# Performance work log

Measured on AMD Instinct MI355X. Metric: run time of the kernel, lower is better.

The kernel has to match this reference:

```python
import jax, jax.numpy as jnp
import numpy as np

EPS = 1e-08  # attention offset, matches module epsilon


def _ln(x, g, b, eps=1e-5):
    m = jnp.mean(x, axis=-1, keepdims=True)
    v = jnp.var(x, axis=-1, keepdims=True)
    return (x - m) * jax.lax.rsqrt(v + eps) * g + b


def setup_inputs() -> dict:
    key = jax.random.key(0)
    ks = jax.random.split(key, 12)
    B, N, D, S, H = 32, 16384, 64, 7, 128
    sc = 1.0 / np.sqrt(D)
    sch = 1.0 / np.sqrt(H)
    return {
        "inputs": jax.random.normal(ks[0], (B, N, D), jnp.float32),
        "ln_in_g": jnp.ones((D,), jnp.float32), "ln_in_b": jnp.zeros((D,), jnp.float32),
        "ln_slots_g": jnp.ones((D,), jnp.float32), "ln_slots_b": jnp.zeros((D,), jnp.float32),
        "ln_mlp_g": jnp.ones((D,), jnp.float32), "ln_mlp_b": jnp.zeros((D,), jnp.float32),
        "Wq": jax.random.normal(ks[1], (D, D), jnp.float32) * sc,
        "Wk": jax.random.normal(ks[2], (D, D), jnp.float32) * sc,
        "Wv": jax.random.normal(ks[3], (D, D), jnp.float32) * sc,
        "slots_mu": jax.random.normal(ks[4], (1, 1, D), jnp.float32),
        "slots_log_sigma": jax.random.normal(ks[5], (1, 1, D), jnp.float32) * 0.1,
        "w_ih": jax.random.normal(ks[6], (3 * D, D), jnp.float32) * sc,
        "w_hh": jax.random.normal(ks[7], (3 * D, D), jnp.float32) * sc,
        "b_ih": jnp.zeros((3 * D,), jnp.float32), "b_hh": jnp.zeros((3 * D,), jnp.float32),
        "mlp_w1": jax.random.normal(ks[8], (H, D), jnp.float32) * sc,
        "mlp_b1": jnp.zeros((H,), jnp.float32),
        "mlp_w2": jax.random.normal(ks[9], (D, H), jnp.float32) * sch,
        "mlp_b2": jnp.zeros((D,), jnp.float32),
        "noise_slots": jax.random.normal(ks[10], (B, S, D), jnp.float32),
        "noise_h": jax.random.normal(ks[11], (B, D), jnp.float32),
        "num_iterations": 3,
    }


def reference(inputs, ln_in_g, ln_in_b, ln_slots_g, ln_slots_b, ln_mlp_g, ln_mlp_b,
              Wq, Wk, Wv, slots_mu, slots_log_sigma, w_ih, w_hh, b_ih, b_hh,
              mlp_w1, mlp_b1, mlp_w2, mlp_b2, noise_slots, noise_h, num_iterations):
    D = inputs.shape[-1]
    scale = D ** -0.5

    x = _ln(inputs, ln_in_g, ln_in_b)               # [B,N,D]
    k = jnp.einsum('bnd,ed->bne', x, Wk)            # [B,N,D]
    v = jnp.einsum('bnd,ed->bne', x, Wv)            # [B,N,D]

    sigma = jnp.exp(slots_log_sigma)
    slots = slots_mu + sigma * noise_slots          # [B,S,D]
    h0 = (slots_mu + sigma * noise_h[None])[0]      # [B,D] (torch h0 is [1,B,D])

    def gru_step(h, x_t):  # torch GRU cell, gate order r,z,n
        gi = x_t @ w_ih.T + b_ih
        gh = h @ w_hh.T + b_hh
        ir, iz, inn = jnp.split(gi, 3, axis=-1)
        hr, hz, hn = jnp.split(gh, 3, axis=-1)
        r = jax.nn.sigmoid(ir + hr)
        z = jax.nn.sigmoid(iz + hz)
        n = jnp.tanh(inn + r * hn)
        h_new = (1.0 - z) * n + z * h
        return h_new, h_new

    for _ in range(num_iterations):
        sn = _ln(slots, ln_slots_g, ln_slots_b)
        q = jnp.einsum('bsd,ed->bse', sn, Wq) * scale        # [B,S,D]
        logits = jnp.einsum('bnd,bsd->bns', k, q)            # [B,N,S]
        attn = jax.nn.softmax(logits, axis=-1) + EPS          # softmax over slots
        attn = attn / jnp.sum(attn, axis=1, keepdims=True)   # normalize over inputs (dim=-2)
        updates = jnp.einsum('bns,bnd->bsd', attn, v)        # [B,S,D]
        # nn.GRU over the slot axis as "time", fixed h0 each iteration
        _, hs = jax.lax.scan(gru_step, h0, jnp.swapaxes(updates, 0, 1))
        slots = jnp.swapaxes(hs, 0, 1)                       # [B,S,D]
        hid = jax.nn.relu(_ln(slots, ln_mlp_g, ln_mlp_b) @ mlp_w1.T + mlp_b1)
        slots = slots + (hid @ mlp_w2.T + mlp_b2)
    return slots
```

## Files before the change

### kernel.cpp

```cpp
#include <hip/hip_runtime.h>
#include <hip/hip_bf16.h>


#define B_ 32
#define N_ 16384
#define D_ 64
#define S_ 7

typedef __bf16 bf16x8 __attribute__((ext_vector_type(8)));
typedef float floatx4 __attribute__((ext_vector_type(4)));

__device__ __forceinline__ unsigned int f2bfu(float f) {
  __hip_bfloat16 h = __float2bfloat16(f);
  return (unsigned int)__builtin_bit_cast(unsigned short, h);
}
__device__ __forceinline__ unsigned int pack2bf(float lo, float hi) {
  return f2bfu(lo) | (f2bfu(hi) << 16);
}

__global__ __launch_bounds__(256) void proj_kernel(
    const float* __restrict__ x,
    const float* __restrict__ lng, const float* __restrict__ lnb,
    const float* __restrict__ Wk, const float* __restrict__ Wv,
    unsigned short* __restrict__ kb, unsigned short* __restrict__ vt)
{
  __shared__ __align__(16) unsigned char smem[32768];
  unsigned short* s_xn = (unsigned short*)smem;
  unsigned short* s_w  = (unsigned short*)(smem + 16384);
  unsigned short* s_ko = (unsigned short*)smem;
  unsigned short* s_vo = (unsigned short*)smem;

  const int t = threadIdx.x, lane = t & 63, w = t >> 6;
  const int R0 = blockIdx.x * 128;
  const int bb = R0 >> 14;
  const int nbase = R0 & (N_ - 1);

#pragma unroll
  for (int p = 0; p < 4; ++p) {
    int idx = (p * 256 + t) * 8;
    const float* src = (idx < 4096) ? (Wk + idx) : (Wv + idx - 4096);
    float4 a = ((const float4*)src)[0], b = ((const float4*)src)[1];
    uint4 pk;
    pk.x = pack2bf(a.x, a.y); pk.y = pack2bf(a.z, a.w);
    pk.z = pack2bf(b.x, b.y); pk.w = pack2bf(b.z, b.w);
    *(uint4*)&s_w[idx] = pk;
  }

  const int ql = t & 3;
  float4 g4[4], b4[4];
#pragma unroll
  for (int j = 0; j < 4; ++j) {
    g4[j] = *(const float4*)&lng[ql * 16 + j * 4];
    b4[j] = *(const float4*)&lnb[ql * 16 + j * 4];
  }
#pragma unroll
  for (int half = 0; half < 2; ++half) {
    int r = half * 64 + (t >> 2);
    const float4* xp = (const float4*)&x[(size_t)(R0 + r) * 64 + ql * 16];
    float4 xv[4];
#pragma unroll
    for (int j = 0; j < 4; ++j) xv[j] = xp[j];
    float s1 = 0.f, s2 = 0.f;
#pragma unroll
    for (int j = 0; j < 4; ++j) {
      s1 += xv[j].x + xv[j].y + xv[j].z + xv[j].w;
      s2 += xv[j].x * xv[j].x + xv[j].y * xv[j].y + xv[j].z * xv[j].z + xv[j].w * xv[j].w;
    }
    s1 += __shfl_xor(s1, 1); s2 += __shfl_xor(s2, 1);
    s1 += __shfl_xor(s1, 2); s2 += __shfl_xor(s2, 2);
    float mean = s1 * 0.015625f;
    float var = s2 * 0.015625f - mean * mean;
    float rs = rsqrtf(var + 1e-5f);
    float y[16];
#pragma unroll
    for (int j = 0; j < 4; ++j) {
      y[j * 4 + 0] = (xv[j].x - mean) * rs * g4[j].x + b4[j].x;
      y[j * 4 + 1] = (xv[j].y - mean) * rs * g4[j].y + b4[j].y;
      y[j * 4 + 2] = (xv[j].z - mean) * rs * g4[j].z + b4[j].z;
      y[j * 4 + 3] = (xv[j].w - mean) * rs * g4[j].w + b4[j].w;
    }
#pragma unroll
    for (int h = 0; h < 2; ++h) {
      uint4 p;
      p.x = pack2bf(y[h * 8 + 0], y[h * 8 + 1]);
      p.y = pack2bf(y[h * 8 + 2], y[h * 8 + 3]);
      p.z = pack2bf(y[h * 8 + 4], y[h * 8 + 5]);
      p.w = pack2bf(y[h * 8 + 6], y[h * 8 + 7]);
      int c = ql * 2 + h;
      int sc = c ^ (r & 7);
      *(uint4*)&s_xn[r * 64 + sc * 8] = p;
    }
  }
  __syncthreads();

  const int m16 = lane & 15, quad = lane >> 4;
  bf16x8 bf[2][2];
#pragma unroll
  for (int rt = 0; rt < 2; ++rt) {
    int xr = (w * 2 + rt) * 16 + m16;
#pragma unroll
    for (int kk = 0; kk < 2; ++kk)
      bf[rt][kk] = *(const bf16x8*)&s_xn[xr * 64 + (((kk * 4 + quad) ^ (xr & 7)) * 8)];
  }
  bf16x8 wkf[4][2], wvf[4][2];
#pragma unroll
  for (int ft = 0; ft < 4; ++ft)
#pragma unroll
    for (int kk = 0; kk < 2; ++kk) {
      wkf[ft][kk] = *(const bf16x8*)&s_w[(ft * 16 + m16) * 64 + kk * 32 + quad * 8];
      wvf[ft][kk] = *(const bf16x8*)&s_w[(64 + ft * 16 + m16) * 64 + kk * 32 + quad * 8];
    }
  __syncthreads();

#pragma unroll
  for (int ft = 0; ft < 4; ++ft)
#pragma unroll
    for (int rt = 0; rt < 2; ++rt) {
      floatx4 acc = (floatx4){0.f, 0.f, 0.f, 0.f};
      acc = __builtin_amdgcn_mfma_f32_16x16x32_bf16(wkf[ft][0], bf[rt][0], acc, 0, 0, 0);
      acc = __builtin_amdgcn_mfma_f32_16x16x32_bf16(wkf[ft][1], bf[rt][1], acc, 0, 0, 0);
      int n_l = (w * 2 + rt) * 16 + m16;
      uint2 p;
      p.x = pack2bf(acc[0], acc[1]);
      p.y = pack2bf(acc[2], acc[3]);
      *(uint2*)&s_ko[n_l * 72 + ft * 16 + quad * 4] = p;
    }
  __syncthreads();
#pragma unroll
  for (int p = 0; p < 4; ++p) {
    int ii = (p * 256 + t) * 8;
    int n_l = ii >> 6, dl = ii & 63;
    uint4 v4 = *(const uint4*)&s_ko[n_l * 72 + dl];
    *(uint4*)&kb[(size_t)(R0 + n_l) * 64 + dl] = v4;
  }
  __syncthreads();

#pragma unroll
  for (int ft = 0; ft < 4; ++ft)
#pragma unroll
    for (int rt = 0; rt < 2; ++rt) {
      floatx4 acc = (floatx4){0.f, 0.f, 0.f, 0.f};
      acc = __builtin_amdgcn_mfma_f32_16x16x32_bf16(bf[rt][0], wvf[ft][0], acc, 0, 0, 0);
      acc = __builtin_amdgcn_mfma_f32_16x16x32_bf16(bf[rt][1], wvf[ft][1], acc, 0, 0, 0);
      int n_l = (w * 2 + rt) * 16 + quad * 4;
      int d0 = ft * 16 + m16;
      uint2 p;
      p.x = pack2bf(acc[0], acc[1]);
      p.y = pack2bf(acc[2], acc[3]);
      *(uint2*)&s_vo[d0 * 136 + n_l] = p;
    }
  __syncthreads();
#pragma unroll
  for (int p = 0; p < 4; ++p) {
    int ii = (p * 256 + t) * 8;
    int d0 = ii >> 7, nl = ii & 127;
    uint4 v4 = *(const uint4*)&s_vo[d0 * 136 + nl];
    *(uint4*)&vt[((size_t)bb * 64 + d0) * N_ + nbase + nl] = v4;
  }
}

__device__ void q_from_slots(const float* s_slot, float* s_tmp,
                             const float* __restrict__ g, const float* __restrict__ bb,
                             const float* __restrict__ Wq, float* __restrict__ qout,
                             int lane, int w)
{
  for (int ss = 0; ss < 2; ++ss) {
    int srow = ss * 4 + w;
    if (srow < 7) {
      float xv = s_slot[srow * 64 + lane];
      float s1 = xv, s2 = xv * xv;
#pragma unroll
      for (int mm = 1; mm < 64; mm <<= 1) {
        s1 += __shfl_xor(s1, mm);
        s2 += __shfl_xor(s2, mm);
      }
      float mean = s1 * 0.015625f;
      float var = s2 * 0.015625f - mean * mean;
      float rs = rsqrtf(var + 1e-5f);
      s_tmp[w * 64 + lane] = (xv - mean) * rs * g[lane] + bb[lane];
    }
    __syncthreads();
    if (srow < 7) {
      float acc = 0.f;
      const float4* wr = (const float4*)(Wq + lane * 64);
      const float4* xr = (const float4*)(s_tmp + w * 64);
#pragma unroll
      for (int i = 0; i < 16; ++i) {
        float4 a = wr[i], xx = xr[i];
        acc += a.x * xx.x + a.y * xx.y + a.z * xx.z + a.w * xx.w;
      }
      qout[srow * 64 + lane] = acc * 0.125f;
    }
    __syncthreads();
  }
}

__global__ __launch_bounds__(256) void init_kernel(
    const float* __restrict__ mu, const float* __restrict__ lsig,
    const float* __restrict__ nslots, const float* __restrict__ nh,
    const float* __restrict__ ln_s_g, const float* __restrict__ ln_s_b,
    const float* __restrict__ Wq,
    float* __restrict__ qbuf, float* __restrict__ h0b)
{
  __shared__ float s_slot[448];
  __shared__ float s_tmp[256];
  const int b = blockIdx.x, t = threadIdx.x, lane = t & 63, w = t >> 6;
  for (int o = t; o < 448; o += 256) {
    int d = o & 63;
    s_slot[o] = mu[d] + expf(lsig[d]) * nslots[b * 448 + o];
  }
  if (t < 64) h0b[b * 64 + t] = mu[t] + expf(lsig[t]) * nh[b * 64 + t];
  __syncthreads();
  q_from_slots(s_slot, s_tmp, ln_s_g, ln_s_b, Wq, qbuf + b * 448, lane, w);
}

__global__ __launch_bounds__(512, 4) void attn_kernel(
    const unsigned short* __restrict__ kb, const unsigned short* __restrict__ vt,
    const float* __restrict__ qbuf,
    float* __restrict__ Wp, float* __restrict__ Cp)
{
  __shared__ __align__(16) unsigned short s_qb[16 * 64];
  __shared__ __align__(16) unsigned short s_at[8][16 * 72];
  __shared__ __align__(16) float s_red[8][448];
  __shared__ float s_cred[8][8];

  const int b = blockIdx.y;
  const int t = threadIdx.x, lane = t & 63, w = t >> 6;
  const int m16 = lane & 15, quad = lane >> 4;

  if (t < 256) {
    int i0 = t * 4;
    int s = i0 >> 6, d0 = i0 & 63;
    float f0 = 0.f, f1 = 0.f, f2 = 0.f, f3 = 0.f;
    if (s < 7) {
      const float* qp = qbuf + b * 448 + s * 64 + d0;
      f0 = qp[0]; f1 = qp[1]; f2 = qp[2]; f3 = qp[3];
    }
    uint2 p;
    p.x = pack2bf(f0, f1);
    p.y = pack2bf(f2, f3);
    *(uint2*)&s_qb[i0] = p;
  }
  __syncthreads();

  bf16x8 bq0 = *(const bf16x8*)&s_qb[m16 * 64 + quad * 8];
  bf16x8 bq1 = *(const bf16x8*)&s_qb[m16 * 64 + 32 + quad * 8];

  const int n0w = blockIdx.x * 512 + w * 64;
  const unsigned short* kbA = kb + ((size_t)b * N_ + n0w) * 64;

  bf16x8 ak[4][2];
#pragma unroll
  for (int nt = 0; nt < 4; ++nt) {
    ak[nt][0] = *(const bf16x8*)&kbA[(size_t)(nt * 16 + m16) * 64 + quad * 8];
    ak[nt][1] = *(const bf16x8*)&kbA[(size_t)(nt * 16 + m16) * 64 + 32 + quad * 8];
  }
  floatx4 cc[4];
#pragma unroll
  for (int nt = 0; nt < 4; ++nt) {
    floatx4 c = (floatx4){0.f, 0.f, 0.f, 0.f};
    c = __builtin_amdgcn_mfma_f32_16x16x32_bf16(ak[nt][0], bq0, c, 0, 0, 0);
    c = __builtin_amdgcn_mfma_f32_16x16x32_bf16(ak[nt][1], bq1, c, 0, 0, 0);
    cc[nt] = c;
  }
  float cl = 0.f;
#pragma unroll
  for (int nt = 0; nt < 4; ++nt) {
    float atv[4];
#pragma unroll
    for (int rg = 0; rg < 4; ++rg) {
      float e = (m16 < 7) ? __expf(cc[nt][rg]) : 0.f;
      float sm = e;
      sm += __shfl_xor(sm, 1);
      sm += __shfl_xor(sm, 2);
      sm += __shfl_xor(sm, 4);
      float a = e * __builtin_amdgcn_rcpf(sm) + 1e-8f;
      atv[rg] = a;
      cl += a;
    }
    if (m16 < 7) {
      uint2 p;
      p.x = pack2bf(atv[0], atv[1]);
      p.y = pack2bf(atv[2], atv[3]);
      *(uint2*)&s_at[w][m16 * 72 + nt * 16 + quad * 4] = p;
    }
  }

  bf16x8 bv[2][4];
  const unsigned short* vtB = vt + (size_t)b * 64 * N_ + n0w;
#pragma unroll
  for (int ch = 0; ch < 2; ++ch)
#pragma unroll
    for (int dt = 0; dt < 4; ++dt)
      bv[ch][dt] = *(const bf16x8*)&vtB[(size_t)(dt * 16 + m16) * N_ + ch * 32 + quad * 8];
  asm volatile("s_waitcnt lgkmcnt(0)" ::: "memory");
  bf16x8 af0 = *(const bf16x8*)&s_at[w][m16 * 72 + quad * 8];
  bf16x8 af1 = *(const bf16x8*)&s_at[w][m16 * 72 + 32 + quad * 8];

  floatx4 acc[4];
#pragma unroll
  for (int dt = 0; dt < 4; ++dt) acc[dt] = (floatx4){0.f, 0.f, 0.f, 0.f};
#pragma unroll
  for (int dt = 0; dt < 4; ++dt)
    acc[dt] = __builtin_amdgcn_mfma_f32_16x16x32_bf16(af0, bv[0][dt], acc[dt], 0, 0, 0);
#pragma unroll
  for (int dt = 0; dt < 4; ++dt)
    acc[dt] = __builtin_amdgcn_mfma_f32_16x16x32_bf16(af1, bv[1][dt], acc[dt], 0, 0, 0);

  if (quad < 2) {
#pragma unroll
    for (int dt = 0; dt < 4; ++dt)
#pragma unroll
      for (int rg = 0; rg < 4; ++rg) {
        int s = quad * 4 + rg;
        if (s < 7) s_red[w][s * 64 + dt * 16 + m16] = acc[dt][rg];
      }
  }
  cl += __shfl_xor(cl, 16);
  cl += __shfl_xor(cl, 32);
  if (m16 < 7 && quad == 0) s_cred[w][m16] = cl;
  __syncthreads();

  if (t < 448) {
    float v = 0.f;
#pragma unroll
    for (int wv = 0; wv < 8; ++wv) v += s_red[wv][t];
    Wp[((size_t)b * 32 + blockIdx.x) * 448 + t] = v;
  } else if (t < 455) {
    int s = t - 448;
    float c = 0.f;
#pragma unroll
    for (int wv = 0; wv < 8; ++wv) c += s_cred[wv][s];
    Cp[((size_t)b * 32 + blockIdx.x) * 8 + s] = c;
  }
}

__global__ __launch_bounds__(256) void slot_update_kernel(
    const float* __restrict__ Wp, const float* __restrict__ Cp,
    const float* __restrict__ h0b,
    const float* __restrict__ w_ih, const float* __restrict__ w_hh,
    const float* __restrict__ b_ih, const float* __restrict__ b_hh,
    const float* __restrict__ ln_m_g, const float* __restrict__ ln_m_b,
    const float* __restrict__ w1, const float* __restrict__ b1,
    const float* __restrict__ w2, const float* __restrict__ b2,
    const float* __restrict__ ln_s_g, const float* __restrict__ ln_s_b,
    const float* __restrict__ Wq,
    float* __restrict__ qbuf, float* __restrict__ out)
{
  const int b = blockIdx.x, t = threadIdx.x, lane = t & 63, w = t >> 6;
  __shared__ float s_whhT[64 * 201];
  __shared__ float s_upd[448];
  __shared__ float s_gi[1344];
  __shared__ float s_h[64];
  __shared__ float s_gh[192];
  __shared__ float s_slot[448];
  __shared__ float s_tmp[256];
  __shared__ float s_cs[8];

  for (int i = t; i < 12288; i += 256) {
    int j = i >> 6, d = i & 63;
    s_whhT[d * 201 + j] = w_hh[i];
  }
  if (t < 7) {
    float cs = 0.f;
#pragma unroll
    for (int p = 0; p < 32; ++p) cs += Cp[((size_t)b * 32 + p) * 8 + t];
    s_cs[t] = cs;
  }
  if (t < 64) s_h[t] = h0b[b * 64 + t];
  __syncthreads();
  for (int o = t; o < 448; o += 256) {
    int s = o >> 6;
    float acc = 0.f;
#pragma unroll
    for (int p = 0; p < 32; ++p) acc += Wp[((size_t)b * 32 + p) * 448 + o];
    s_upd[o] = acc / s_cs[s];
  }
  __syncthreads();
  for (int o = t; o < 1344; o += 256) {
    int s = o / 192, j = o - s * 192;
    float acc = b_ih[j];
    const float4* wr = (const float4*)(w_ih + j * 64);
    const float4* ur = (const float4*)(s_upd + s * 64);
#pragma unroll
    for (int i = 0; i < 16; ++i) {
      float4 a = wr[i], u = ur[i];
      acc += a.x * u.x + a.y * u.y + a.z * u.z + a.w * u.w;
    }
    s_gi[o] = acc;
  }
  __syncthreads();
  for (int s = 0; s < 7; ++s) {
    if (t < 192) {
      float acc = b_hh[t];
#pragma unroll 16
      for (int d = 0; d < 64; ++d) acc += s_h[d] * s_whhT[d * 201 + t];
      s_gh[t] = acc;
    }
    __syncthreads();
    if (t < 64) {
      float ir = s_gi[s * 192 + t], iz = s_gi[s * 192 + 64 + t], inn = s_gi[s * 192 + 128 + t];
      float hr = s_gh[t], hz = s_gh[64 + t], hn = s_gh[128 + t];
      float r = 1.f / (1.f + expf(-(ir + hr)));
      float z = 1.f / (1.f + expf(-(iz + hz)));
      float n = tanhf(inn + r * hn);
      float hnew = (1.f - z) * n + z * s_h[t];
      s_slot[s * 64 + t] = hnew;
      s_h[t] = hnew;
    }
    __syncthreads();
  }
  float* s_sn = s_gi;
  float* s_hid = s_gi + 448;
  for (int ss = 0; ss < 2; ++ss) {
    int srow = ss * 4 + w;
    if (srow < 7) {
      float xv = s_slot[srow * 64 + lane];
      float s1 = xv, s2 = xv * xv;
#pragma unroll
      for (int mm = 1; mm < 64; mm <<= 1) {
        s1 += __shfl_xor(s1, mm);
        s2 += __shfl_xor(s2, mm);
      }
      float mean = s1 * 0.015625f;
      float var = s2 * 0.015625f - mean * mean;
      float rs = rsqrtf(var + 1e-5f);
      s_sn[srow * 64 + lane] = (xv - mean) * rs * ln_m_g[lane] + ln_m_b[lane];
    }
  }
  __syncthreads();
  for (int o = t; o < 896; o += 256) {
    int s = o >> 7, hh = o & 127;
    float acc = b1[hh];
    const float4* wr = (const float4*)(w1 + hh * 64);
    const float4* xr = (const float4*)(s_sn + s * 64);
#pragma unroll
    for (int i = 0; i < 16; ++i) {
      float4 a = wr[i], xx = xr[i];
      acc += a.x * xx.x + a.y * xx.y + a.z * xx.z + a.w * xx.w;
    }
    s_hid[o] = fmaxf(acc, 0.f);
  }
  __syncthreads();
  for (int o = t; o < 448; o += 256) {
    int s = o >> 6, d = o & 63;
    float acc = b2[d];
    const float4* wr = (const float4*)(w2 + d * 128);
    const float4* hr = (const float4*)(s_hid + s * 128);
#pragma unroll
    for (int i = 0; i < 32; ++i) {
      float4 a = wr[i], hv = hr[i];
      acc += a.x * hv.x + a.y * hv.y + a.z * hv.z + a.w * hv.w;
    }
    float val = s_slot[o] + acc;
    s_slot[o] = val;
    out[b * 448 + o] = val;
  }
  __syncthreads();
  q_from_slots(s_slot, s_tmp, ln_s_g, ln_s_b, Wq, qbuf + b * 448, lane, w);
}

extern "C" void kernel_launch(void* const* d_in, const int* in_sizes, int n_in,
                              void* d_out, int out_size, void* d_ws, size_t ws_size,
                              hipStream_t stream)
{
  (void)in_sizes; (void)n_in; (void)out_size; (void)ws_size;
  const float* x      = (const float*)d_in[0];
  const float* ln_in_g = (const float*)d_in[1];
  const float* ln_in_b = (const float*)d_in[2];
  const float* ln_s_g  = (const float*)d_in[3];
  const float* ln_s_b  = (const float*)d_in[4];
  const float* ln_m_g  = (const float*)d_in[5];
  const float* ln_m_b  = (const float*)d_in[6];
  const float* Wq = (const float*)d_in[7];
  const float* Wk = (const float*)d_in[8];
  const float* Wv = (const float*)d_in[9];
  const float* mu = (const float*)d_in[10];
  const float* lsig = (const float*)d_in[11];
  const float* w_ih = (const float*)d_in[12];
  const float* w_hh = (const float*)d_in[13];
  const float* b_ih = (const float*)d_in[14];
  const float* b_hh = (const float*)d_in[15];
  const float* w1 = (const float*)d_in[16];
  const float* b1 = (const float*)d_in[17];
  const float* w2 = (const float*)d_in[18];
  const float* b2 = (const float*)d_in[19];
  const float* nslots = (const float*)d_in[20];
  const float* nh = (const float*)d_in[21];

  unsigned short* kb = (unsigned short*)d_ws;
  unsigned short* vt = kb + (size_t)B_ * N_ * D_;
  float* fb = (float*)(vt + (size_t)B_ * N_ * D_);
  float* qbuf = fb;
  float* h0b  = fb + 14336;
  float* Wp   = fb + 16384;
  float* Cp   = Wp + 458752;
  float* out = (float*)d_out;

  proj_kernel<<<4096, 256, 0, stream>>>(x, ln_in_g, ln_in_b, Wk, Wv, kb, vt);
  init_kernel<<<32, 256, 0, stream>>>(mu, lsig, nslots, nh, ln_s_g, ln_s_b, Wq,
                                      qbuf, h0b);
  for (int it = 0; it < 3; ++it) {
    attn_kernel<<<dim3(32, 32), 512, 0, stream>>>(kb, vt, qbuf, Wp, Cp);
    slot_update_kernel<<<32, 256, 0, stream>>>(Wp, Cp, h0b, w_ih, w_hh, b_ih, b_hh,
                                               ln_m_g, ln_m_b, w1, b1, w2, b2,
                                               ln_s_g, ln_s_b, Wq, qbuf, out);
  }
}
```

Baseline: 424.6 us.

## Fuse first attention iteration into projection kernel, pre-convert weights to bf16

The first slot-attention iteration (logits, softmax over slots, attention-weighted V partial sums) is now computed inside the K/V projection kernel from tiles already in shared memory. This removes one full re-read of K and V from global memory. Wk/Wv are converted to bf16 once in init_kernel instead of in every projection block. The slot update kernel is widened to 512 threads, takes a variable partial count, and uses flags so the last iteration skips the query computation and earlier iterations skip the output write. The projection kernel now does more work and uses more shared memory per block, and the first reduction reads 128 partials per batch instead of 32.

```diff
diff --git a/kernel.cpp b/kernel.cpp
--- a/kernel.cpp
+++ b/kernel.cpp
@@ -18,32 +18,103 @@
   return f2bfu(lo) | (f2bfu(hi) << 16);
 }
 
-__global__ __launch_bounds__(256) void proj_kernel(
+__device__ void q_from_slots(const float* s_slot, float* s_tmp,
+                             const float* __restrict__ g, const float* __restrict__ bb,
+                             const float* __restrict__ Wq, float* __restrict__ qout,
+                             int lane, int w)
+{
+  for (int ss = 0; ss < 2; ++ss) {
+    int srow = ss * 4 + w;
+    if (srow < 7) {
+      float xv = s_slot[srow * 64 + lane];
+      float s1 = xv, s2 = xv * xv;
+#pragma unroll
+      for (int mm = 1; mm < 64; mm <<= 1) {
+        s1 += __shfl_xor(s1, mm);
+        s2 += __shfl_xor(s2, mm);
+      }
+      float mean = s1 * 0.015625f;
+      float var = s2 * 0.015625f - mean * mean;
+      float rs = rsqrtf(var + 1e-5f);
+      s_tmp[w * 64 + lane] = (xv - mean) * rs * g[lane] + bb[lane];
+    }
+    __syncthreads();
+    if (srow < 7) {
+      float acc = 0.f;
+      const float4* wr = (const float4*)(Wq + lane * 64);
+      const float4* xr = (const float4*)(s_tmp + w * 64);
+#pragma unroll
+      for (int i = 0; i < 16; ++i) {
+        float4 a = wr[i], xx = xr[i];
+        acc += a.x * xx.x + a.y * xx.y + a.z * xx.z + a.w * xx.w;
+      }
+      qout[srow * 64 + lane] = acc * 0.125f;
+    }
+    __syncthreads();
+  }
+}
+
+__global__ __launch_bounds__(256) void init_kernel(
+    const float* __restrict__ mu, const float* __restrict__ lsig,
+    const float* __restrict__ nslots, const float* __restrict__ nh,
+    const float* __restrict__ ln_s_g, const float* __restrict__ ln_s_b,
+    const float* __restrict__ Wq,
+    const float* __restrict__ Wk, const float* __restrict__ Wv,
+    float* __restrict__ qbuf, float* __restrict__ h0b,
+    unsigned short* __restrict__ wkb, unsigned short* __restrict__ wvb)
+{
+  __shared__ float s_slot[448];
+  __shared__ float s_tmp[256];
+  const int b = blockIdx.x, t = threadIdx.x, lane = t & 63, w = t >> 6;
+  {
+    int gid = b * 256 + t;
+    if (gid < 4096) wkb[gid] = (unsigned short)f2bfu(Wk[gid]);
+    else            wvb[gid - 4096] = (unsigned short)f2bfu(Wv[gid - 4096]);
+  }
+  for (int o = t; o < 448; o += 256) {
+    int d = o & 63;
+    s_slot[o] = mu[d] + expf(lsig[d]) * nslots[b * 448 + o];
+  }
+  if (t < 64) h0b[b * 64 + t] = mu[t] + expf(lsig[t]) * nh[b * 64 + t];
+  __syncthreads();
+  q_from_slots(s_slot, s_tmp, ln_s_g, ln_s_b, Wq, qbuf + b * 448, lane, w);
+}
+
+__global__ __launch_bounds__(256, 4) void proj_kernel(
     const float* __restrict__ x,
     const float* __restrict__ lng, const float* __restrict__ lnb,
-    const float* __restrict__ Wk, const float* __restrict__ Wv,
-    unsigned short* __restrict__ kb, unsigned short* __restrict__ vt)
+    const unsigned short* __restrict__ wkb, const unsigned short* __restrict__ wvb,
+    const float* __restrict__ qbuf,
+    unsigned short* __restrict__ kb, unsigned short* __restrict__ vt,
+    float* __restrict__ Wp, float* __restrict__ Cp)
 {
-  __shared__ __align__(16) unsigned char smem[32768];
-  unsigned short* s_xn = (unsigned short*)smem;
-  unsigned short* s_w  = (unsigned short*)(smem + 16384);
-  unsigned short* s_ko = (unsigned short*)smem;
-  unsigned short* s_vo = (unsigned short*)smem;
+  __shared__ __align__(16) unsigned char smemA[18432];
+  __shared__ __align__(16) unsigned short s_vo[64 * 136];
+  __shared__ __align__(16) unsigned short s_qb[1024];
+  __shared__ float s_cred[4][8];
+  unsigned short* s_xn = (unsigned short*)smemA;
+  unsigned short* s_ko = (unsigned short*)smemA;
+  unsigned short* s_at = (unsigned short*)smemA;
+  float* s_red = (float*)(smemA + 5120);
 
   const int t = threadIdx.x, lane = t & 63, w = t >> 6;
   const int R0 = blockIdx.x * 128;
   const int bb = R0 >> 14;
   const int nbase = R0 & (N_ - 1);
-
-#pragma unroll
-  for (int p = 0; p < 4; ++p) {
-    int idx = (p * 256 + t) * 8;
-    const float* src = (idx < 4096) ? (Wk + idx) : (Wv + idx - 4096);
-    float4 a = ((const float4*)src)[0], b = ((const float4*)src)[1];
-    uint4 pk;
-    pk.x = pack2bf(a.x, a.y); pk.y = pack2bf(a.z, a.w);
-    pk.z = pack2bf(b.x, b.y); pk.w = pack2bf(b.z, b.w);
-    *(uint4*)&s_w[idx] = pk;
+  const int chunk = nbase >> 7;
+
+  {
+    int i0 = t * 4;
+    int s = i0 >> 6, d0 = i0 & 63;
+    float f0 = 0.f, f1 = 0.f, f2 = 0.f, f3 = 0.f;
+    if (s < 7) {
+      const float* qp = qbuf + bb * 448 + s * 64 + d0;
+      f0 = qp[0]; f1 = qp[1]; f2 = qp[2]; f3 = qp[3];
+    }
+    uint2 p;
+    p.x = pack2bf(f0, f1);
+    p.y = pack2bf(f2, f3);
+    *(uint2*)&s_qb[i0] = p;
   }
 
   const int ql = t & 3;
@@ -94,6 +165,9 @@
   __syncthreads();
 
   const int m16 = lane & 15, quad = lane >> 4;
+  bf16x8 bq0 = *(const bf16x8*)&s_qb[m16 * 64 + quad * 8];
+  bf16x8 bq1 = *(const bf16x8*)&s_qb[m16 * 64 + 32 + quad * 8];
+
   bf16x8 bf[2][2];
 #pragma unroll
   for (int rt = 0; rt < 2; ++rt) {
@@ -107,8 +181,8 @@
   for (int ft = 0; ft < 4; ++ft)
 #pragma unroll
     for (int kk = 0; kk < 2; ++kk) {
-      wkf[ft][kk] = *(const bf16x8*)&s_w[(ft * 16 + m16) * 64 + kk * 32 + quad * 8];
-      wvf[ft][kk] = *(const bf16x8*)&s_w[(64 + ft * 16 + m16) * 64 + kk * 32 + quad * 8];
+      wkf[ft][kk] = *(const bf16x8*)&wkb[(ft * 16 + m16) * 64 + kk * 32 + quad * 8];
+      wvf[ft][kk] = *(const bf16x8*)&wvb[(ft * 16 + m16) * 64 + kk * 32 + quad * 8];
     }
   __syncthreads();
 
@@ -125,14 +199,6 @@
       p.y = pack2bf(acc[2], acc[3]);
       *(uint2*)&s_ko[n_l * 72 + ft * 16 + quad * 4] = p;
     }
-  __syncthreads();
-#pragma unroll
-  for (int p = 0; p < 4; ++p) {
-    int ii = (p * 256 + t) * 8;
-    int n_l = ii >> 6, dl = ii & 63;
-    uint4 v4 = *(const uint4*)&s_ko[n_l * 72 + dl];
-    *(uint4*)&kb[(size_t)(R0 + n_l) * 64 + dl] = v4;
-  }
   __syncthreads();
 
 #pragma unroll
@@ -149,7 +215,79 @@
       p.y = pack2bf(acc[2], acc[3]);
       *(uint2*)&s_vo[d0 * 136 + n_l] = p;
     }
-  __syncthreads();
+  bf16x8 ak[2][2];
+#pragma unroll
+  for (int rt = 0; rt < 2; ++rt) {
+    int row = (w * 2 + rt) * 16 + m16;
+    ak[rt][0] = *(const bf16x8*)&s_ko[row * 72 + quad * 8];
+    ak[rt][1] = *(const bf16x8*)&s_ko[row * 72 + 32 + quad * 8];
+  }
+#pragma unroll
+  for (int p = 0; p < 4; ++p) {
+    int ii = (p * 256 + t) * 8;
+    int n_l = ii >> 6, dl = ii & 63;
+    uint4 v4 = *(const uint4*)&s_ko[n_l * 72 + dl];
+    *(uint4*)&kb[(size_t)(R0 + n_l) * 64 + dl] = v4;
+  }
+  __syncthreads();
+
+  float cl = 0.f;
+#pragma unroll
+  for (int rt = 0; rt < 2; ++rt) {
+    floatx4 c = (floatx4){0.f, 0.f, 0.f, 0.f};
+    c = __builtin_amdgcn_mfma_f32_16x16x32_bf16(ak[rt][0], bq0, c, 0, 0, 0);
+    c = __builtin_amdgcn_mfma_f32_16x16x32_bf16(ak[rt][1], bq1, c, 0, 0, 0);
+    float atv[4];
+#pragma unroll
+    for (int rg = 0; rg < 4; ++rg) {
+      float e = (m16 < 7) ? __expf(c[rg]) : 0.f;
+      float sm = e;
+      sm += __shfl_xor(sm, 1);
+      sm += __shfl_xor(sm, 2);
+      sm += __shfl_xor(sm, 4);
+      float a = e * __builtin_amdgcn_rcpf(sm) + 1e-8f;
+      atv[rg] = a;
+      cl += a;
+    }
+    if (m16 < 7) {
+      uint2 p;
+      p.x = pack2bf(atv[0], atv[1]);
+      p.y = pack2bf(atv[2], atv[3]);
+      *(uint2*)&s_at[w * 640 + m16 * 40 + rt * 16 + quad * 4] = p;
+    }
+  }
+  asm volatile("s_waitcnt lgkmcnt(0)" ::: "memory");
+  bf16x8 af = *(const bf16x8*)&s_at[w * 640 + m16 * 40 + quad * 8];
+  floatx4 acc2[4];
+#pragma unroll
+  for (int dt = 0; dt < 4; ++dt) acc2[dt] = (floatx4){0.f, 0.f, 0.f, 0.f};
+#pragma unroll
+  for (int dt = 0; dt < 4; ++dt) {
+    bf16x8 bv = *(const bf16x8*)&s_vo[(dt * 16 + m16) * 136 + w * 32 + quad * 8];
+    acc2[dt] = __builtin_amdgcn_mfma_f32_16x16x32_bf16(af, bv, acc2[dt], 0, 0, 0);
+  }
+  if (quad < 2) {
+#pragma unroll
+    for (int dt = 0; dt < 4; ++dt)
+#pragma unroll
+      for (int rg = 0; rg < 4; ++rg) {
+        int s = quad * 4 + rg;
+        if (s < 7) s_red[w * 448 + s * 64 + dt * 16 + m16] = acc2[dt][rg];
+      }
+  }
+  cl += __shfl_xor(cl, 16);
+  cl += __shfl_xor(cl, 32);
+  if (m16 < 7 && quad == 0) s_cred[w][m16] = cl;
+  __syncthreads();
+
+  for (int o = t; o < 448; o += 256) {
+    float v = s_red[o] + s_red[448 + o] + s_red[896 + o] + s_red[1344 + o];
+    Wp[((size_t)bb * 128 + chunk) * 448 + o] = v;
+  }
+  if (t < 7) {
+    float c = s_cred[0][t] + s_cred[1][t] + s_cred[2][t] + s_cred[3][t];
+    Cp[((size_t)bb * 128 + chunk) * 8 + t] = c;
+  }
 #pragma unroll
   for (int p = 0; p < 4; ++p) {
     int ii = (p * 256 + t) * 8;
@@ -157,61 +295,6 @@
     uint4 v4 = *(const uint4*)&s_vo[d0 * 136 + nl];
     *(uint4*)&vt[((size_t)bb * 64 + d0) * N_ + nbase + nl] = v4;
   }
-}
-
-__device__ void q_from_slots(const float* s_slot, float* s_tmp,
-                             const float* __restrict__ g, const float* __restrict__ bb,
-                             const float* __restrict__ Wq, float* __restrict__ qout,
-                             int lane, int w)
-{
-  for (int ss = 0; ss < 2; ++ss) {
-    int srow = ss * 4 + w;
-    if (srow < 7) {
-      float xv = s_slot[srow * 64 + lane];
-      float s1 = xv, s2 = xv * xv;
-#pragma unroll
-      for (int mm = 1; mm < 64; mm <<= 1) {
-        s1 += __shfl_xor(s1, mm);
-        s2 += __shfl_xor(s2, mm);
-      }
-      float mean = s1 * 0.015625f;
-      float var = s2 * 0.015625f - mean * mean;
-      float rs = rsqrtf(var + 1e-5f);
-      s_tmp[w * 64 + lane] = (xv - mean) * rs * g[lane] + bb[lane];
-    }
-    __syncthreads();
-    if (srow < 7) {
-      float acc = 0.f;
-      const float4* wr = (const float4*)(Wq + lane * 64);
-      const float4* xr = (const float4*)(s_tmp + w * 64);
-#pragma unroll
-      for (int i = 0; i < 16; ++i) {
-        float4 a = wr[i], xx = xr[i];
-        acc += a.x * xx.x + a.y * xx.y + a.z * xx.z + a.w * xx.w;
-      }
-      qout[srow * 64 + lane] = acc * 0.125f;
-    }
-    __syncthreads();
-  }
-}
-
-__global__ __launch_bounds__(256) void init_kernel(
-    const float* __restrict__ mu, const float* __restrict__ lsig,
-    const float* __restrict__ nslots, const float* __restrict__ nh,
-    const float* __restrict__ ln_s_g, const float* __restrict__ ln_s_b,
-    const float* __restrict__ Wq,
-    float* __restrict__ qbuf, float* __restrict__ h0b)
-{
-  __shared__ float s_slot[448];
-  __shared__ float s_tmp[256];
-  const int b = blockIdx.x, t = threadIdx.x, lane = t & 63, w = t >> 6;
-  for (int o = t; o < 448; o += 256) {
-    int d = o & 63;
-    s_slot[o] = mu[d] + expf(lsig[d]) * nslots[b * 448 + o];
-  }
-  if (t < 64) h0b[b * 64 + t] = mu[t] + expf(lsig[t]) * nh[b * 64 + t];
-  __syncthreads();
-  q_from_slots(s_slot, s_tmp, ln_s_g, ln_s_b, Wq, qbuf + b * 448, lane, w);
 }
 
 __global__ __launch_bounds__(512, 4) void attn_kernel(
@@ -335,8 +418,8 @@
   }
 }
 
-__global__ __launch_bounds__(256) void slot_update_kernel(
-    const float* __restrict__ Wp, const float* __restrict__ Cp,
+__global__ __launch_bounds__(512) void slot_update_kernel(
+    const float* __restrict__ Wp, const float* __restrict__ Cp, int npart,
     const float* __restrict__ h0b,
     const float* __restrict__ w_ih, const float* __restrict__ w_hh,
     const float* __restrict__ b_ih, const float* __restrict__ b_hh,
@@ -345,7 +428,7 @@
     const float* __restrict__ w2, const float* __restrict__ b2,
     const float* __restrict__ ln_s_g, const float* __restrict__ ln_s_b,
     const float* __restrict__ Wq,
-    float* __restrict__ qbuf, float* __restrict__ out)
+    float* __restrict__ qbuf, float* __restrict__ out, int flags)
 {
   const int b = blockIdx.x, t = threadIdx.x, lane = t & 63, w = t >> 6;
   __shared__ float s_whhT[64 * 201];
@@ -354,30 +437,29 @@
   __shared__ float s_h[64];
   __shared__ float s_gh[192];
   __shared__ float s_slot[448];
-  __shared__ float s_tmp[256];
+  __shared__ float s_tmp[512];
   __shared__ float s_cs[8];
 
-  for (int i = t; i < 12288; i += 256) {
+  for (int i = t; i < 12288; i += 512) {
     int j = i >> 6, d = i & 63;
     s_whhT[d * 201 + j] = w_hh[i];
   }
   if (t < 7) {
     float cs = 0.f;
-#pragma unroll
-    for (int p = 0; p < 32; ++p) cs += Cp[((size_t)b * 32 + p) * 8 + t];
+#pragma unroll 8
+    for (int p = 0; p < npart; ++p) cs += Cp[((size_t)b * npart + p) * 8 + t];
     s_cs[t] = cs;
   }
   if (t < 64) s_h[t] = h0b[b * 64 + t];
   __syncthreads();
-  for (int o = t; o < 448; o += 256) {
-    int s = o >> 6;
+  if (t < 448) {
     float acc = 0.f;
-#pragma unroll
-    for (int p = 0; p < 32; ++p) acc += Wp[((size_t)b * 32 + p) * 448 + o];
-    s_upd[o] = acc / s_cs[s];
-  }
-  __syncthreads();
-  for (int o = t; o < 1344; o += 256) {
+#pragma unroll 8
+    for (int p = 0; p < npart; ++p) acc += Wp[((size_t)b * npart + p) * 448 + t];
+    s_upd[t] = acc / s_cs[t >> 6];
+  }
+  __syncthreads();
+  for (int o = t; o < 1344; o += 512) {
     int s = o / 192, j = o - s * 192;
     float acc = b_ih[j];
     const float4* wr = (const float4*)(w_ih + j * 64);
@@ -412,10 +494,51 @@
   }
   float* s_sn = s_gi;
   float* s_hid = s_gi + 448;
-  for (int ss = 0; ss < 2; ++ss) {
-    int srow = ss * 4 + w;
-    if (srow < 7) {
-      float xv = s_slot[srow * 64 + lane];
+  if (w < 7) {
+    float xv = s_slot[w * 64 + lane];
+    float s1 = xv, s2 = xv * xv;
+#pragma unroll
+    for (int mm = 1; mm < 64; mm <<= 1) {
+      s1 += __shfl_xor(s1, mm);
+      s2 += __shfl_xor(s2, mm);
+    }
+    float mean = s1 * 0.015625f;
+    float var = s2 * 0.015625f - mean * mean;
+    float rs = rsqrtf(var + 1e-5f);
+    s_sn[w * 64 + lane] = (xv - mean) * rs * ln_m_g[lane] + ln_m_b[lane];
+  }
+  __syncthreads();
+  for (int o = t; o < 896; o += 512) {
+    int s = o >> 7, hh = o & 127;
+    float acc = b1[hh];
+    const float4* wr = (const float4*)(w1 + hh * 64);
+    const float4* xr = (const float4*)(s_sn + s * 64);
+#pragma unroll
+    for (int i = 0; i < 16; ++i) {
+      float4 a = wr[i], xx = xr[i];
+      acc += a.x * xx.x + a.y * xx.y + a.z * xx.z + a.w * xx.w;
+    }
+    s_hid[o] = fmaxf(acc, 0.f);
+  }
+  __syncthreads();
+  for (int o = t; o < 448; o += 512) {
+    int s = o >> 6, d = o & 63;
+    float acc = b2[d];
+    const float4* wr = (const float4*)(w2 + d * 128);
+    const float4* hr = (const float4*)(s_hid + s * 128);
+#pragma unroll
+    for (int i = 0; i < 32; ++i) {
+      float4 a = wr[i], hv = hr[i];
+      acc += a.x * hv.x + a.y * hv.y + a.z * hv.z + a.w * hv.w;
+    }
+    float val = s_slot[o] + acc;
+    s_slot[o] = val;
+    if (flags & 1) out[b * 448 + o] = val;
+  }
+  __syncthreads();
+  if (flags & 2) {
+    if (w < 7) {
+      float xv = s_slot[w * 64 + lane];
       float s1 = xv, s2 = xv * xv;
 #pragma unroll
       for (int mm = 1; mm < 64; mm <<= 1) {
@@ -425,39 +548,21 @@
       float mean = s1 * 0.015625f;
       float var = s2 * 0.015625f - mean * mean;
       float rs = rsqrtf(var + 1e-5f);
-      s_sn[srow * 64 + lane] = (xv - mean) * rs * ln_m_g[lane] + ln_m_b[lane];
-    }
-  }
-  __syncthreads();
-  for (int o = t; o < 896; o += 256) {
-    int s = o >> 7, hh = o & 127;
-    float acc = b1[hh];
-    const float4* wr = (const float4*)(w1 + hh * 64);
-    const float4* xr = (const float4*)(s_sn + s * 64);
-#pragma unroll
-    for (int i = 0; i < 16; ++i) {
-      float4 a = wr[i], xx = xr[i];
-      acc += a.x * xx.x + a.y * xx.y + a.z * xx.z + a.w * xx.w;
-    }
-    s_hid[o] = fmaxf(acc, 0.f);
-  }
-  __syncthreads();
-  for (int o = t; o < 448; o += 256) {
-    int s = o >> 6, d = o & 63;
-    float acc = b2[d];
-    const float4* wr = (const float4*)(w2 + d * 128);
-    const float4* hr = (const float4*)(s_hid + s * 128);
-#pragma unroll
-    for (int i = 0; i < 32; ++i) {
-      float4 a = wr[i], hv = hr[i];
-      acc += a.x * hv.x + a.y * hv.y + a.z * hv.z + a.w * hv.w;
-    }
-    float val = s_slot[o] + acc;
-    s_slot[o] = val;
-    out[b * 448 + o] = val;
-  }
-  __syncthreads();
-  q_from_slots(s_slot, s_tmp, ln_s_g, ln_s_b, Wq, qbuf + b * 448, lane, w);
+      s_tmp[w * 64 + lane] = (xv - mean) * rs * ln_s_g[lane] + ln_s_b[lane];
+    }
+    __syncthreads();
+    if (w < 7) {
+      float acc = 0.f;
+      const float4* wr = (const float4*)(Wq + lane * 64);
+      const float4* xr = (const float4*)(s_tmp + w * 64);
+#pragma unroll
+      for (int i = 0; i < 16; ++i) {
+        float4 a = wr[i], xx = xr[i];
+        acc += a.x * xx.x + a.y * xx.y + a.z * xx.z + a.w * xx.w;
+      }
+      qbuf[b * 448 + w * 64 + lane] = acc * 0.125f;
+    }
+  }
 }
 
 extern "C" void kernel_launch(void* const* d_in, const int* in_sizes, int n_in,
@@ -488,22 +593,29 @@
   const float* nslots = (const float*)d_in[20];
   const float* nh = (const float*)d_in[21];
 
-  unsigned short* kb = (unsigned short*)d_ws;
-  unsigned short* vt = kb + (size_t)B_ * N_ * D_;
-  float* fb = (float*)(vt + (size_t)B_ * N_ * D_);
+  unsigned short* kb  = (unsigned short*)d_ws;
+  unsigned short* vt  = kb + (size_t)B_ * N_ * D_;
+  unsigned short* wkb = vt + (size_t)B_ * N_ * D_;
+  unsigned short* wvb = wkb + 4096;
+  float* fb  = (float*)(wvb + 4096);
   float* qbuf = fb;
   float* h0b  = fb + 14336;
   float* Wp   = fb + 16384;
-  float* Cp   = Wp + 458752;
+  float* Cp   = Wp + 1835008;
   float* out = (float*)d_out;
 
-  proj_kernel<<<4096, 256, 0, stream>>>(x, ln_in_g, ln_in_b, Wk, Wv, kb, vt);
   init_kernel<<<32, 256, 0, stream>>>(mu, lsig, nslots, nh, ln_s_g, ln_s_b, Wq,
-                                      qbuf, h0b);
-  for (int it = 0; it < 3; ++it) {
-    attn_kernel<<<dim3(32, 32), 512, 0, stream>>>(kb, vt, qbuf, Wp, Cp);
-    slot_update_kernel<<<32, 256, 0, stream>>>(Wp, Cp, h0b, w_ih, w_hh, b_ih, b_hh,
-                                               ln_m_g, ln_m_b, w1, b1, w2, b2,
-                                               ln_s_g, ln_s_b, Wq, qbuf, out);
-  }
-}
+                                      Wk, Wv, qbuf, h0b, wkb, wvb);
+  proj_kernel<<<4096, 256, 0, stream>>>(x, ln_in_g, ln_in_b, wkb, wvb, qbuf, kb, vt, Wp, Cp);
+  slot_update_kernel<<<32, 512, 0, stream>>>(Wp, Cp, 128, h0b, w_ih, w_hh, b_ih, b_hh,
+                                             ln_m_g, ln_m_b, w1, b1, w2, b2,
+                                             ln_s_g, ln_s_b, Wq, qbuf, out, 2);
+  attn_kernel<<<dim3(32, 32), 512, 0, stream>>>(kb, vt, qbuf, Wp, Cp);
+  slot_update_kernel<<<32, 512, 0, stream>>>(Wp, Cp, 32, h0b, w_ih, w_hh, b_ih, b_hh,
+                                             ln_m_g, ln_m_b, w1, b1, w2, b2,
+                                             ln_s_g, ln_s_b, Wq, qbuf, out, 2);
+  attn_kernel<<<dim3(32, 32), 512, 0, stream>>>(kb, vt, qbuf, Wp, Cp);
+  slot_update_kernel<<<32, 512, 0, stream>>>(Wp, Cp, 32, h0b, w_ih, w_hh, b_ih, b_hh,
+                                             ln_m_g, ln_m_b, w1, b1, w2, b2,
+                                             ln_s_g, ln_s_b, Wq, qbuf, out, 1);
+}
```

New measurement: 427.0 us. Within noise of the previous version (+0.6%).
